# Performance work log

Measured on AMD Instinct MI355X. Metric: run time of the kernel, lower is better.

The kernel has to match this reference:

```python
import jax, jax.numpy as jnp
import numpy as np

GAMMA = 0.5  # matches init_kwargs gamma

def setup_inputs() -> dict:
    key = jax.random.key(0)
    kx, km = jax.random.split(key)
    x = jax.random.normal(kx, (65536, 64), dtype=jnp.float32)
    # keras 'uniform' initializer draws from U(-0.05, 0.05)
    mu = jax.random.uniform(km, (64, 256), dtype=jnp.float32, minval=-0.05, maxval=0.05)
    return {"x": x, "mu": mu}

def reference(x, mu):
    # Original: l2[b,u] = sum_d (x[b,d] - mu[d,u])^2 ; out = exp(-gamma * l2)
    x_sq = jnp.sum(x * x, axis=-1, keepdims=True)           # (B, 1)
    mu_sq = jnp.sum(mu * mu, axis=0)[None, :]               # (1, U)
    cross = jnp.einsum('bd,du->bu', x, mu)                  # (B, U)
    l2 = x_sq - 2.0 * cross + mu_sq                          # (B, U)
    return jnp.exp(-GAMMA * l2)
```

## Files before the change

### kernel.cpp

```cpp
#include <hip/hip_runtime.h>
#include <hip/hip_bf16.h>


typedef __attribute__((ext_vector_type(8))) short short8;
typedef __attribute__((ext_vector_type(4))) float floatx4;

__device__ inline short f2bf_rne(float f) {
    unsigned int u = __float_as_uint(f);
    u += 0x7fffu + ((u >> 16) & 1u);
    return (short)(u >> 16);
}

__global__ __launch_bounds__(256, 4) void rbf_kernel(
    const float* __restrict__ x, const float* __restrict__ mu,
    float* __restrict__ out, int nRowTiles, int gridBlocks)
{
    const int tid  = threadIdx.x;
    const int wave = tid >> 6;
    const int lane = tid & 63;
    const int l15  = lane & 15;
    const int g    = lane >> 4;

    short8 bfrag[4][2];
    float  msq[4];
    const int ubase = wave * 64;
    #pragma unroll
    for (int t = 0; t < 4; ++t) {
        const int u = ubase + t * 16 + l15;
        float sq = 0.f;
        #pragma unroll
        for (int h = 0; h < 2; ++h) {
            short8 bf;
            const int k0 = 32 * h + 8 * g;
            #pragma unroll
            for (int e = 0; e < 8; ++e) {
                float v = mu[(k0 + e) * 256 + u];
                sq += v * v;
                bf[e] = f2bf_rne(v);
            }
            bfrag[t][h] = bf;
        }
        sq += __shfl_xor(sq, 16);
        sq += __shfl_xor(sq, 32);
        msq[t] = -0.5f * sq;
    }

    for (int rt = blockIdx.x; rt < nRowTiles; rt += gridBlocks) {
        const int b0 = rt * 16;
        const float* xr = x + (size_t)(b0 + l15) * 64 + 8 * g;
        floatx4 v0 = *(const floatx4*)(xr);
        floatx4 v1 = *(const floatx4*)(xr + 4);
        floatx4 v2 = *(const floatx4*)(xr + 32);
        floatx4 v3 = *(const floatx4*)(xr + 36);

        short8 afrag[2];
        float xsq = 0.f;
        #pragma unroll
        for (int e = 0; e < 4; ++e) {
            xsq += v0[e] * v0[e] + v1[e] * v1[e];
            xsq += v2[e] * v2[e] + v3[e] * v3[e];
            afrag[0][e]     = f2bf_rne(v0[e]);
            afrag[0][e + 4] = f2bf_rne(v1[e]);
            afrag[1][e]     = f2bf_rne(v2[e]);
            afrag[1][e + 4] = f2bf_rne(v3[e]);
        }
        xsq += __shfl_xor(xsq, 16);
        xsq += __shfl_xor(xsq, 32);
        float xh[4];
        #pragma unroll
        for (int r = 0; r < 4; ++r)
            xh[r] = -0.5f * __shfl(xsq, 4 * g + r);

        #pragma unroll
        for (int t = 0; t < 4; ++t) {
            floatx4 acc = {0.f, 0.f, 0.f, 0.f};
            acc = __builtin_amdgcn_mfma_f32_16x16x32_bf16(afrag[0], bfrag[t][0], acc, 0, 0, 0);
            acc = __builtin_amdgcn_mfma_f32_16x16x32_bf16(afrag[1], bfrag[t][1], acc, 0, 0, 0);
            const int u = ubase + t * 16 + l15;
            #pragma unroll
            for (int r = 0; r < 4; ++r) {
                float arg = acc[r] + xh[r] + msq[t];
                out[(size_t)(b0 + 4 * g + r) * 256 + u] = __expf(arg);
            }
        }
    }
}

extern "C" void kernel_launch(void* const* d_in, const int* in_sizes, int n_in,
                              void* d_out, int out_size, void* d_ws, size_t ws_size,
                              hipStream_t stream) {
    const float* x  = (const float*)d_in[0];
    const float* mu = (const float*)d_in[1];
    float* out = (float*)d_out;
    const int nRowTiles = 65536 / 16;
    const int gridBlocks = 2048;
    hipLaunchKernelGGL(rbf_kernel, dim3(gridBlocks), dim3(256), 0, stream,
                       x, mu, out, nRowTiles, gridBlocks);
}
```

Before: 92.01 us.

## Prefetch next x tile, use nontemporal loads/stores, halve grid with unrolled tiles

Halves the grid to 1024 blocks, each handling exactly four row tiles in a fully unrolled loop. The next tile's x data is loaded before the current tile is computed, so loads overlap with MFMA and exp work. Loads of x and stores of the output use nontemporal hints to reduce cache pollution on this write-heavy kernel. The trip count is hardcoded to the fixed problem size and adds register pressure from the prefetch buffers.

```diff
diff --git a/kernel.cpp b/kernel.cpp
--- a/kernel.cpp
+++ b/kernel.cpp
@@ -5,25 +5,32 @@
 typedef __attribute__((ext_vector_type(8))) short short8;
 typedef __attribute__((ext_vector_type(4))) float floatx4;
 
+#define GRIDB 1024
+#define TILES 4
+
 __device__ inline short f2bf_rne(float f) {
     unsigned int u = __float_as_uint(f);
     u += 0x7fffu + ((u >> 16) & 1u);
     return (short)(u >> 16);
 }
 
+__device__ inline floatx4 ldnt4(const float* p) {
+    return __builtin_nontemporal_load((const floatx4*)p);
+}
+
 __global__ __launch_bounds__(256, 4) void rbf_kernel(
     const float* __restrict__ x, const float* __restrict__ mu,
-    float* __restrict__ out, int nRowTiles, int gridBlocks)
+    float* __restrict__ out)
 {
     const int tid  = threadIdx.x;
     const int wave = tid >> 6;
     const int lane = tid & 63;
     const int l15  = lane & 15;
     const int g    = lane >> 4;
+    const int ubase = wave * 64;
 
     short8 bfrag[4][2];
     float  msq[4];
-    const int ubase = wave * 64;
     #pragma unroll
     for (int t = 0; t < 4; ++t) {
         const int u = ubase + t * 16 + l15;
@@ -45,24 +52,30 @@
         msq[t] = -0.5f * sq;
     }
 
-    for (int rt = blockIdx.x; rt < nRowTiles; rt += gridBlocks) {
-        const int b0 = rt * 16;
-        const float* xr = x + (size_t)(b0 + l15) * 64 + 8 * g;
-        floatx4 v0 = *(const floatx4*)(xr);
-        floatx4 v1 = *(const floatx4*)(xr + 4);
-        floatx4 v2 = *(const floatx4*)(xr + 32);
-        floatx4 v3 = *(const floatx4*)(xr + 36);
+    int rt = blockIdx.x;
+    const float* xr0 = x + (size_t)(rt * 16 + l15) * 64 + 8 * g;
+    floatx4 c0 = ldnt4(xr0), c1 = ldnt4(xr0 + 4),
+            c2 = ldnt4(xr0 + 32), c3 = ldnt4(xr0 + 36);
 
-        short8 afrag[2];
+    #pragma unroll
+    for (int i = 0; i < TILES; ++i) {
+        floatx4 n0, n1, n2, n3;
+        if (i + 1 < TILES) {
+            const float* xn = x + (size_t)((rt + GRIDB) * 16 + l15) * 64 + 8 * g;
+            n0 = ldnt4(xn); n1 = ldnt4(xn + 4);
+            n2 = ldnt4(xn + 32); n3 = ldnt4(xn + 36);
+        }
+
+        short8 a0, a1;
         float xsq = 0.f;
         #pragma unroll
         for (int e = 0; e < 4; ++e) {
-            xsq += v0[e] * v0[e] + v1[e] * v1[e];
-            xsq += v2[e] * v2[e] + v3[e] * v3[e];
-            afrag[0][e]     = f2bf_rne(v0[e]);
-            afrag[0][e + 4] = f2bf_rne(v1[e]);
-            afrag[1][e]     = f2bf_rne(v2[e]);
-            afrag[1][e + 4] = f2bf_rne(v3[e]);
+            xsq += c0[e] * c0[e] + c1[e] * c1[e];
+            xsq += c2[e] * c2[e] + c3[e] * c3[e];
+            a0[e]     = f2bf_rne(c0[e]);
+            a0[e + 4] = f2bf_rne(c1[e]);
+            a1[e]     = f2bf_rne(c2[e]);
+            a1[e + 4] = f2bf_rne(c3[e]);
         }
         xsq += __shfl_xor(xsq, 16);
         xsq += __shfl_xor(xsq, 32);
@@ -71,17 +84,24 @@
         for (int r = 0; r < 4; ++r)
             xh[r] = -0.5f * __shfl(xsq, 4 * g + r);
 
+        const int b0 = rt * 16;
         #pragma unroll
         for (int t = 0; t < 4; ++t) {
             floatx4 acc = {0.f, 0.f, 0.f, 0.f};
-            acc = __builtin_amdgcn_mfma_f32_16x16x32_bf16(afrag[0], bfrag[t][0], acc, 0, 0, 0);
-            acc = __builtin_amdgcn_mfma_f32_16x16x32_bf16(afrag[1], bfrag[t][1], acc, 0, 0, 0);
+            acc = __builtin_amdgcn_mfma_f32_16x16x32_bf16(a0, bfrag[t][0], acc, 0, 0, 0);
+            acc = __builtin_amdgcn_mfma_f32_16x16x32_bf16(a1, bfrag[t][1], acc, 0, 0, 0);
             const int u = ubase + t * 16 + l15;
             #pragma unroll
             for (int r = 0; r < 4; ++r) {
                 float arg = acc[r] + xh[r] + msq[t];
-                out[(size_t)(b0 + 4 * g + r) * 256 + u] = __expf(arg);
+                __builtin_nontemporal_store(__expf(arg),
+                    &out[(size_t)(b0 + 4 * g + r) * 256 + u]);
             }
+        }
+
+        if (i + 1 < TILES) {
+            c0 = n0; c1 = n1; c2 = n2; c3 = n3;
+            rt += GRIDB;
         }
     }
 }
@@ -92,8 +112,5 @@
     const float* x  = (const float*)d_in[0];
     const float* mu = (const float*)d_in[1];
     float* out = (float*)d_out;
-    const int nRowTiles = 65536 / 16;
-    const int gridBlocks = 2048;
-    hipLaunchKernelGGL(rbf_kernel, dim3(gridBlocks), dim3(256), 0, stream,
-                       x, mu, out, nRowTiles, gridBlocks);
+    hipLaunchKernelGGL(rbf_kernel, dim3(GRIDB), dim3(256), 0, stream, x, mu, out);
 }
```

Result: slower. 105.0 us (+14.2%).
